# Optimization experiments

Measured on AMD Instinct MI355X. Metric: run time of the kernel, lower is better.

## Reference

```python
import jax, jax.numpy as jnp
import numpy as np

HIDDEN = 256
MSG = 256
N_CLASSES = 2


def _ggnn(x, adj, W_lin, b_lin, W_ih, b_ih, W_hh, b_hh, n_timesteps):
    # Append supernode: zero-embedding row to h, ones row + zeros col to adj.
    N = x.shape[0]
    h0 = jnp.concatenate([x, jnp.zeros((1, x.shape[1]), x.dtype)], axis=0)  # [N+1, H]
    A = jnp.concatenate([adj, jnp.ones((1, N), adj.dtype)], axis=0)         # [N+1, N]
    A = jnp.concatenate([A, jnp.zeros((N + 1, 1), adj.dtype)], axis=1)      # [N+1, N+1]

    def step(h, _):
        msgs = h @ W_lin.T + b_lin          # [N+1, MSG] linear projection
        m = A @ msgs                        # [N+1, MSG] message aggregation
        # GRUCell (PyTorch convention): gates order r, z, n
        gi = m @ W_ih.T + b_ih              # [N+1, 3H]
        gh = h @ W_hh.T + b_hh              # [N+1, 3H]
        ir, iz, inn = jnp.split(gi, 3, axis=-1)
        hr, hz, hn = jnp.split(gh, 3, axis=-1)
        r = jax.nn.sigmoid(ir + hr)
        z = jax.nn.sigmoid(iz + hz)
        n = jnp.tanh(inn + r * hn)
        h_new = (1.0 - z) * n + z * h
        return h_new, None

    h, _ = jax.lax.scan(step, h0, None, length=n_timesteps)
    return h


def setup_inputs() -> dict:
    key = jax.random.key(0)
    ks = jax.random.split(key, 12)
    N = 8000
    inp = {
        "b_x": jax.random.normal(ks[0], (N, HIDDEN), dtype=jnp.float32),
        "b_adj": (jax.random.uniform(ks[1], (N, N), dtype=jnp.float32) < 0.002).astype(jnp.float32),
        "a_x": jax.random.normal(ks[2], (N, HIDDEN), dtype=jnp.float32),
        "a_adj": (jax.random.uniform(ks[3], (N, N), dtype=jnp.float32) < 0.002).astype(jnp.float32),
        "W_lin": jax.random.normal(ks[4], (MSG, HIDDEN), dtype=jnp.float32) * 0.05,
        "b_lin": jnp.zeros((MSG,), dtype=jnp.float32),
        "W_ih": jax.random.normal(ks[5], (3 * HIDDEN, MSG), dtype=jnp.float32) * 0.05,
        "b_ih": jnp.zeros((3 * HIDDEN,), dtype=jnp.float32),
        "W_hh": jax.random.normal(ks[6], (3 * HIDDEN, HIDDEN), dtype=jnp.float32) * 0.05,
        "b_hh": jnp.zeros((3 * HIDDEN,), dtype=jnp.float32),
        "W_fc": jax.random.normal(ks[7], (N_CLASSES, 2 * HIDDEN), dtype=jnp.float32) * 0.05,
        "b_fc": jnp.zeros((N_CLASSES,), dtype=jnp.float32),
        "n_timesteps": 8,
    }
    return inp


def reference(b_x, b_adj, a_x, a_adj, W_lin, b_lin, W_ih, b_ih, W_hh, b_hh, W_fc, b_fc, n_timesteps):
    b_h = _ggnn(b_x, b_adj, W_lin, b_lin, W_ih, b_ih, W_hh, b_hh, n_timesteps)
    a_h = _ggnn(a_x, a_adj, W_lin, b_lin, W_ih, b_ih, W_hh, b_hh, n_timesteps)
    supernodes = jnp.concatenate([b_h[-1, :], a_h[-1, :]], axis=0)  # [2H]
    logits = supernodes @ W_fc.T + b_fc                              # [n_classes]
    return jax.nn.log_softmax(logits, axis=0)
```

## Files before the change

### kernel.cpp

```cpp
#include <hip/hip_runtime.h>
#include <hip/hip_bf16.h>
#include <math.h>

#define NNODES 8000
#define NP1    8001
#define H      256
#define CAP    64
#define TSTEPS 8
#define MTOT   (2*NP1)
#define MPAD   16128
#define NRB    (MPAD/32)

typedef __attribute__((ext_vector_type(8))) short short8;
typedef __attribute__((ext_vector_type(4))) float floatx4;

__device__ __forceinline__ float bl2f(unsigned short u) {
  union { unsigned int i; float f; } z; z.i = ((unsigned int)u) << 16; return z.f;
}
__device__ __forceinline__ unsigned short f2bl(float f) {
  __hip_bfloat16 b = __float2bfloat16(f);
  return *(unsigned short*)&b;
}
__device__ __forceinline__ float sigf(float x) { return 1.f / (1.f + __expf(-x)); }
__device__ __forceinline__ float tanhf_fast(float x) { return 2.f / (1.f + __expf(-2.f * x)) - 1.f; }

__global__ __launch_bounds__(256) void build_ell_kernel(
    const float* __restrict__ adj_b, const float* __restrict__ adj_a,
    int* __restrict__ counts, int* __restrict__ colidx)
{
  int w = threadIdx.x >> 6, l = threadIdx.x & 63;
  int b = blockIdx.x * 4 + w;
  int g = b >= NNODES;
  int row = b - g * NNODES;
  const float* adj = (g ? adj_a : adj_b) + (size_t)row * NNODES;
  unsigned long long lt = (1ull << l) - 1;
  int base = 0;
  int* dst = colidx + (size_t)b * CAP;

  #define SLOT(vec, u, colv) { \
    bool nz = (&vec.x)[u] != 0.f; \
    unsigned long long m = __ballot(nz); \
    if (nz) { int idx = base + (int)__popcll(m & lt); if (idx < CAP) dst[idx] = (colv); } \
    base += (int)__popcll(m); }
  #define GROUP(vec, cb) { \
    bool any4 = ((&vec.x)[0] != 0.f) | ((&vec.x)[1] != 0.f) | \
                ((&vec.x)[2] != 0.f) | ((&vec.x)[3] != 0.f); \
    if (__ballot(any4)) { \
      SLOT(vec, 0, (cb) + 0) SLOT(vec, 1, (cb) + 1) \
      SLOT(vec, 2, (cb) + 2) SLOT(vec, 3, (cb) + 3) } }

  for (int c0 = l * 4; c0 < NNODES; c0 += 1024) {
    int c1 = c0 + 256, c2 = c0 + 512, c3 = c0 + 768;
    bool p1 = c1 < NNODES, p2 = c2 < NNODES, p3 = c3 < NNODES;
    float4 v0 = *(const float4*)(adj + c0);
    float4 v1 = p1 ? *(const float4*)(adj + c1) : make_float4(0,0,0,0);
    float4 v2 = p2 ? *(const float4*)(adj + c2) : make_float4(0,0,0,0);
    float4 v3 = p3 ? *(const float4*)(adj + c3) : make_float4(0,0,0,0);
    GROUP(v0, c0) GROUP(v1, c1) GROUP(v2, c2) GROUP(v3, c3)
  }
  #undef GROUP
  #undef SLOT
  if (l == 0) counts[b] = base < CAP ? base : CAP;
}

__global__ __launch_bounds__(256) void degf_kernel(
    const int* __restrict__ counts, float* __restrict__ degf)
{
  int row = blockIdx.x * 256 + threadIdx.x;
  float d = 0.f;
  if (row < MTOT) {
    int g = row >= NP1;
    int r = row - g * NP1;
    if (r < NNODES) d = (float)counts[g * NNODES + r];
    else if (r == NNODES) d = (float)NNODES;
  }
  degf[row] = d;
}

__global__ __launch_bounds__(256) void weights_kernel(
    const float* __restrict__ Wih, const float* __restrict__ Wlin,
    const float* __restrict__ blin, const float* __restrict__ Whh,
    __hip_bfloat16* __restrict__ Wbig2, float* __restrict__ bc)
{
  __shared__ float srow[H];
  __shared__ float red[256];
  int p = blockIdx.x;
  int ct32 = p / 96, w96 = p - ct32 * 96;
  int gb = w96 >> 4, u = w96 & 15;
  int jj = gb >> 1, uh = gb & 1;
  int c = ct32 * 32 + uh * 16 + u;
  int gr = jj * 256 + c;
  int t = threadIdx.x;
  size_t ob = (size_t)p * 512;
  srow[t] = Wih[(size_t)gr * H + t];
  __syncthreads();
  float acc = 0.f;
  #pragma unroll 8
  for (int k = 0; k < H; ++k) acc += srow[k] * Wlin[(size_t)k * H + t];
  Wbig2[ob + t] = __float2bfloat16(acc);
  Wbig2[ob + 256 + t] = __float2bfloat16(Whh[(size_t)gr * H + t]);
  red[t] = srow[t] * blin[t];
  __syncthreads();
  for (int s = 128; s > 0; s >>= 1) { if (t < s) red[t] += red[t + s]; __syncthreads(); }
  if (t == 0) bc[gr] = red[0];
}

__global__ __launch_bounds__(256) void init_h_kernel(
    const float* __restrict__ bx, const float* __restrict__ ax,
    float* __restrict__ h, __hip_bfloat16* __restrict__ hbf, float* __restrict__ cs0)
{
  int b = blockIdx.x;
  int t = threadIdx.x;
  float l0 = 0.f, l1 = 0.f;
  for (int q = 0; q < 32; ++q) {
    int row = b * 32 + q;
    int g = row >= NP1;
    int r = row - g * NP1;
    float v = 0.f;
    if (r < NNODES) {
      v = (g ? ax : bx)[(size_t)r * H + t];
      if (g) l1 += v; else l0 += v;
    }
    size_t off = (size_t)row * H + t;
    h[off] = v;
    hbf[off] = __float2bfloat16(v);
  }
  if (l0 != 0.f) atomicAdd(&cs0[t], l0);
  if (l1 != 0.f) atomicAdd(&cs0[256 + t], l1);
}

__global__ __launch_bounds__(256) void spmm_kernel(
    const unsigned short* __restrict__ hbf, unsigned short* __restrict__ haggbf,
    const int* __restrict__ counts, const int* __restrict__ colidx,
    const float* __restrict__ cs)
{
  int w = threadIdx.x >> 6, l = threadIdx.x & 63;
  int b = blockIdx.x * 4 + w;
  if (b >= MTOT) return;
  int g = b >= NP1;
  int r = b - g * NP1;
  size_t outoff = (size_t)b * H + l * 4;
  if (r == NNODES) {
    float4 v = *(const float4*)&cs[g * H + l * 4];
    ushort4 o; o.x = f2bl(v.x); o.y = f2bl(v.y); o.z = f2bl(v.z); o.w = f2bl(v.w);
    *(ushort4*)(haggbf + outoff) = o;
    return;
  }
  int rb = g * NNODES + r;
  int cnt = counts[rb];
  const int* cols = colidx + (size_t)rb * CAP;
  const unsigned short* hg = hbf + (size_t)g * NP1 * H;
  float a0 = 0.f, a1 = 0.f, a2 = 0.f, a3 = 0.f;
  int k = 0;
  for (; k + 4 <= cnt; k += 4) {
    int c0 = cols[k], c1 = cols[k+1], c2 = cols[k+2], c3 = cols[k+3];
    uint2 x0 = *(const uint2*)(hg + (size_t)c0 * H + l * 4);
    uint2 x1 = *(const uint2*)(hg + (size_t)c1 * H + l * 4);
    uint2 x2 = *(const uint2*)(hg + (size_t)c2 * H + l * 4);
    uint2 x3 = *(const uint2*)(hg + (size_t)c3 * H + l * 4);
    a0 += bl2f(x0.x & 0xffff) + bl2f(x1.x & 0xffff) + bl2f(x2.x & 0xffff) + bl2f(x3.x & 0xffff);
    a1 += bl2f(x0.x >> 16)    + bl2f(x1.x >> 16)    + bl2f(x2.x >> 16)    + bl2f(x3.x >> 16);
    a2 += bl2f(x0.y & 0xffff) + bl2f(x1.y & 0xffff) + bl2f(x2.y & 0xffff) + bl2f(x3.y & 0xffff);
    a3 += bl2f(x0.y >> 16)    + bl2f(x1.y >> 16)    + bl2f(x2.y >> 16)    + bl2f(x3.y >> 16);
  }
  for (; k < cnt; ++k) {
    uint2 x = *(const uint2*)(hg + (size_t)cols[k] * H + l * 4);
    a0 += bl2f(x.x & 0xffff); a1 += bl2f(x.x >> 16);
    a2 += bl2f(x.y & 0xffff); a3 += bl2f(x.y >> 16);
  }
  ushort4 o; o.x = f2bl(a0); o.y = f2bl(a1); o.z = f2bl(a2); o.w = f2bl(a3);
  *(ushort4*)(haggbf + outoff) = o;
}

__global__ __launch_bounds__(256, 2) void fused_gemm_gru_kernel(
    const __hip_bfloat16* __restrict__ haggbf, const __hip_bfloat16* __restrict__ hin,
    const __hip_bfloat16* __restrict__ Wbig2, const float* __restrict__ degf,
    const float* __restrict__ bc, const float* __restrict__ bih,
    const float* __restrict__ bhh,
    float* __restrict__ h, __hip_bfloat16* __restrict__ hout,
    float* __restrict__ cs_next)
{
  __shared__ __align__(16) short lsA[256 * 32];
  __shared__ __align__(16) short lsB[96 * 32];
  int bidx = blockIdx.x;
  int ct = bidx >> 6;
  int m_i = bidx & 63;
  if (m_i >= 63) return;
  int m0 = m_i * 256;
  const short* Bbase = (const short*)Wbig2 + (size_t)ct * 96 * 512;
  int t = threadIdx.x;
  int w = t >> 6, l = t & 63;
  int lr = l >> 2, lc = l & 3;
  int wm = (w & 1) * 128, uh = w >> 1;
  int q = l >> 4, lm = l & 15;
  floatx4 acc[8][4] = {};

  for (int k0 = 0; k0 < 512; k0 += 32) {
    bool ihalf = (k0 < 256);
    const short* Asrc = ihalf ? (const short*)haggbf : (const short*)hin;
    int ka = k0 & 255;
    #pragma unroll
    for (int j = 0; j < 4; ++j) {
      int r = w * 64 + j * 16 + lr;
      int cch = lc ^ ((r >> 1) & 3);
      const short* ga = Asrc + (size_t)(m0 + r) * H + ka + cch * 8;
      short* la = lsA + (w * 64 + j * 16) * 32;
      __builtin_amdgcn_global_load_lds((const __attribute__((address_space(1))) void*)ga,
                                       (__attribute__((address_space(3))) void*)la, 16, 0, 0);
    }
    if (w < 3) {
      #pragma unroll
      for (int j = 0; j < 2; ++j) {
        int r = (w * 2 + j) * 16 + lr;
        int cch = lc ^ ((r >> 1) & 3);
        const short* gb = Bbase + (size_t)r * 512 + k0 + cch * 8;
        short* lb = lsB + (w * 2 + j) * 16 * 32;
        __builtin_amdgcn_global_load_lds((const __attribute__((address_space(1))) void*)gb,
                                         (__attribute__((address_space(3))) void*)lb, 16, 0, 0);
      }
    }
    __syncthreads();
    short8 bfr[3];
    #pragma unroll
    for (int jj = 0; jj < 3; ++jj) {
      int n = (jj * 2 + uh) * 16 + lm;
      bfr[jj] = *(const short8*)&lsB[n * 32 + (q ^ ((n >> 1) & 3)) * 8];
    }
    #pragma unroll
    for (int i = 0; i < 8; ++i) {
      int m = wm + i * 16 + lm;
      short8 af = *(const short8*)&lsA[m * 32 + (q ^ ((m >> 1) & 3)) * 8];
      acc[i][0] = __builtin_amdgcn_mfma_f32_16x16x32_bf16(af, bfr[0], acc[i][0], 0, 0, 0);
      acc[i][1] = __builtin_amdgcn_mfma_f32_16x16x32_bf16(af, bfr[1], acc[i][1], 0, 0, 0);
      if (ihalf)
        acc[i][2] = __builtin_amdgcn_mfma_f32_16x16x32_bf16(af, bfr[2], acc[i][2], 0, 0, 0);
      else
        acc[i][3] = __builtin_amdgcn_mfma_f32_16x16x32_bf16(af, bfr[2], acc[i][3], 0, 0, 0);
    }
    __syncthreads();
  }

  int c = ct * 32 + uh * 16 + lm;
  float bcr = bc[c], bcz = bc[256 + c], bcn = bc[512 + c];
  float br  = bih[c] + bhh[c];
  float bz  = bih[256 + c] + bhh[256 + c];
  float bin = bih[512 + c];
  float bhn = bhh[512 + c];
  float lu0 = 0.f, lu1 = 0.f;
  #pragma unroll
  for (int i = 0; i < 8; ++i) {
    int row0 = m0 + wm + i * 16 + q * 4;
    float4 dg = *(const float4*)&degf[row0];
    #pragma unroll
    for (int reg = 0; reg < 4; ++reg) {
      int row = row0 + reg;
      float deg = (&dg.x)[reg];
      float rg = sigf(acc[i][0][reg] + deg * bcr + br);
      float z  = sigf(acc[i][1][reg] + deg * bcz + bz);
      float n  = tanhf_fast(acc[i][2][reg] + deg * bcn + bin + rg * (acc[i][3][reg] + bhn));
      size_t hoff = (size_t)row * H + c;
      float hp = h[hoff];
      float hnew = (1.f - z) * n + z * hp;
      h[hoff] = hnew;
      hout[hoff] = __float2bfloat16(hnew);
      if (row < NP1) { if (row < NNODES) lu0 += hnew; }
      else { if (row - NP1 < NNODES) lu1 += hnew; }
    }
  }
  lu0 += __shfl_down(lu0, 32); lu0 += __shfl_down(lu0, 16);
  lu1 += __shfl_down(lu1, 32); lu1 += __shfl_down(lu1, 16);
  if (q == 0) {
    if (lu0 != 0.f) atomicAdd(&cs_next[c], lu0);
    if (lu1 != 0.f) atomicAdd(&cs_next[256 + c], lu1);
  }
}

__global__ __launch_bounds__(256) void final_kernel(
    const float* __restrict__ h, const float* __restrict__ Wfc,
    const float* __restrict__ bfc, float* __restrict__ out)
{
  __shared__ float red0[256];
  __shared__ float red1[256];
  int t = threadIdx.x;
  float sn0 = h[(size_t)NNODES * H + t];
  float sn1 = h[((size_t)NP1 + NNODES) * H + t];
  red0[t] = sn0 * Wfc[t]       + sn1 * Wfc[H + t];
  red1[t] = sn0 * Wfc[512 + t] + sn1 * Wfc[512 + H + t];
  __syncthreads();
  for (int s = 128; s > 0; s >>= 1) {
    if (t < s) { red0[t] += red0[t + s]; red1[t] += red1[t + s]; }
    __syncthreads();
  }
  if (t == 0) {
    float l0 = red0[0] + bfc[0], l1 = red1[0] + bfc[1];
    float m = fmaxf(l0, l1);
    float lse = m + logf(expf(l0 - m) + expf(l1 - m));
    out[0] = l0 - lse;
    out[1] = l1 - lse;
  }
}

extern "C" void kernel_launch(void* const* d_in, const int* in_sizes, int n_in,
                              void* d_out, int out_size, void* d_ws, size_t ws_size,
                              hipStream_t stream) {
  const float* b_x   = (const float*)d_in[0];
  const float* b_adj = (const float*)d_in[1];
  const float* a_x   = (const float*)d_in[2];
  const float* a_adj = (const float*)d_in[3];
  const float* Wlin  = (const float*)d_in[4];
  const float* blin  = (const float*)d_in[5];
  const float* Wih   = (const float*)d_in[6];
  const float* bih   = (const float*)d_in[7];
  const float* Whh   = (const float*)d_in[8];
  const float* bhh   = (const float*)d_in[9];
  const float* Wfc   = (const float*)d_in[10];
  const float* bfc   = (const float*)d_in[11];
  float* out = (float*)d_out;

  char* ws = (char*)d_ws;
  size_t off = 0;
  auto alloc = [&](size_t bytes) {
    void* p = ws + off;
    off += (bytes + 255) & ~(size_t)255;
    return p;
  };
  float* h               = (float*)alloc((size_t)MPAD * H * 4);
  __hip_bfloat16* hbf0   = (__hip_bfloat16*)alloc((size_t)MPAD * H * 2);
  __hip_bfloat16* hbf1   = (__hip_bfloat16*)alloc((size_t)MPAD * H * 2);
  __hip_bfloat16* haggbf = (__hip_bfloat16*)alloc((size_t)MPAD * H * 2);
  __hip_bfloat16* Wbig2  = (__hip_bfloat16*)alloc((size_t)768 * 512 * 2);
  float* bc              = (float*)alloc((size_t)768 * 4);
  int* colidx            = (int*)alloc((size_t)2 * NNODES * CAP * 4);
  int* counts            = (int*)alloc((size_t)2 * NNODES * 4 + 1024);
  float* degf            = (float*)alloc((size_t)MPAD * 4);
  float* cs              = (float*)alloc((size_t)(TSTEPS + 1) * 2 * H * 4);

  hipMemsetAsync(cs, 0, (size_t)(TSTEPS + 1) * 2 * H * 4, stream);

  build_ell_kernel<<<4000, 256, 0, stream>>>(b_adj, a_adj, counts, colidx);
  degf_kernel<<<MPAD / 256, 256, 0, stream>>>(counts, degf);
  weights_kernel<<<768, 256, 0, stream>>>(Wih, Wlin, blin, Whh, Wbig2, bc);
  init_h_kernel<<<NRB, 256, 0, stream>>>(b_x, a_x, h, hbf0, cs);

  __hip_bfloat16* ping[2] = { hbf0, hbf1 };
  for (int t = 0; t < TSTEPS; ++t) {
    __hip_bfloat16* hin  = ping[t & 1];
    __hip_bfloat16* hout = ping[(t + 1) & 1];
    spmm_kernel<<<(MTOT + 3) / 4, 256, 0, stream>>>(
        (const unsigned short*)hin, (unsigned short*)haggbf, counts, colidx, cs + t * 2 * H);
    fused_gemm_gru_kernel<<<512, 256, 0, stream>>>(
        haggbf, hin, Wbig2, degf, bc, bih, bhh, h, hout, cs + (t + 1) * 2 * H);
  }
  final_kernel<<<1, 256, 0, stream>>>(h, Wfc, bfc, out);
}
```

Before: 911.9 us.

## Double-buffer LDS in fused GEMM and broadcast neighbor indices via shuffles

Converts the fused GEMM+GRU kernel's K loop to a two-stage LDS double buffer: the next tile is loaded while the current one is computed, and one barrier per iteration is removed. In the gather kernel, each lane loads one column index up front and the indices are broadcast with wave shuffles instead of repeated scalar loads. The change doubles LDS use and relies on barrier waitcnt semantics for correctness; the shuffle path assumes cnt <= 64.

```diff
diff --git a/kernel.cpp b/kernel.cpp
--- a/kernel.cpp
+++ b/kernel.cpp
@@ -149,11 +149,13 @@
   int rb = g * NNODES + r;
   int cnt = counts[rb];
   const int* cols = colidx + (size_t)rb * CAP;
+  int c_l = (l < cnt) ? cols[l] : 0;
   const unsigned short* hg = hbf + (size_t)g * NP1 * H;
   float a0 = 0.f, a1 = 0.f, a2 = 0.f, a3 = 0.f;
   int k = 0;
   for (; k + 4 <= cnt; k += 4) {
-    int c0 = cols[k], c1 = cols[k+1], c2 = cols[k+2], c3 = cols[k+3];
+    int c0 = __shfl(c_l, k), c1 = __shfl(c_l, k + 1);
+    int c2 = __shfl(c_l, k + 2), c3 = __shfl(c_l, k + 3);
     uint2 x0 = *(const uint2*)(hg + (size_t)c0 * H + l * 4);
     uint2 x1 = *(const uint2*)(hg + (size_t)c1 * H + l * 4);
     uint2 x2 = *(const uint2*)(hg + (size_t)c2 * H + l * 4);
@@ -164,7 +166,8 @@
     a3 += bl2f(x0.y >> 16)    + bl2f(x1.y >> 16)    + bl2f(x2.y >> 16)    + bl2f(x3.y >> 16);
   }
   for (; k < cnt; ++k) {
-    uint2 x = *(const uint2*)(hg + (size_t)cols[k] * H + l * 4);
+    int c = __shfl(c_l, k);
+    uint2 x = *(const uint2*)(hg + (size_t)c * H + l * 4);
     a0 += bl2f(x.x & 0xffff); a1 += bl2f(x.x >> 16);
     a2 += bl2f(x.y & 0xffff); a3 += bl2f(x.y >> 16);
   }
@@ -180,14 +183,16 @@
     float* __restrict__ h, __hip_bfloat16* __restrict__ hout,
     float* __restrict__ cs_next)
 {
-  __shared__ __align__(16) short lsA[256 * 32];
-  __shared__ __align__(16) short lsB[96 * 32];
+  __shared__ __align__(16) short lsA[2][256 * 32];
+  __shared__ __align__(16) short lsB[2][96 * 32];
   int bidx = blockIdx.x;
   int ct = bidx >> 6;
   int m_i = bidx & 63;
   if (m_i >= 63) return;
   int m0 = m_i * 256;
   const short* Bbase = (const short*)Wbig2 + (size_t)ct * 96 * 512;
+  const short* Ai = (const short*)haggbf;
+  const short* Ah = (const short*)hin;
   int t = threadIdx.x;
   int w = t >> 6, l = t & 63;
   int lr = l >> 2, lc = l & 3;
@@ -195,41 +200,49 @@
   int q = l >> 4, lm = l & 15;
   floatx4 acc[8][4] = {};
 
-  for (int k0 = 0; k0 < 512; k0 += 32) {
-    bool ihalf = (k0 < 256);
-    const short* Asrc = ihalf ? (const short*)haggbf : (const short*)hin;
-    int ka = k0 & 255;
-    #pragma unroll
-    for (int j = 0; j < 4; ++j) {
-      int r = w * 64 + j * 16 + lr;
-      int cch = lc ^ ((r >> 1) & 3);
-      const short* ga = Asrc + (size_t)(m0 + r) * H + ka + cch * 8;
-      short* la = lsA + (w * 64 + j * 16) * 32;
-      __builtin_amdgcn_global_load_lds((const __attribute__((address_space(1))) void*)ga,
-                                       (__attribute__((address_space(3))) void*)la, 16, 0, 0);
-    }
-    if (w < 3) {
-      #pragma unroll
-      for (int j = 0; j < 2; ++j) {
-        int r = (w * 2 + j) * 16 + lr;
-        int cch = lc ^ ((r >> 1) & 3);
-        const short* gb = Bbase + (size_t)r * 512 + k0 + cch * 8;
-        short* lb = lsB + (w * 2 + j) * 16 * 32;
-        __builtin_amdgcn_global_load_lds((const __attribute__((address_space(1))) void*)gb,
-                                         (__attribute__((address_space(3))) void*)lb, 16, 0, 0);
-      }
-    }
+  #define STAGE(ks) { \
+    int buf_ = (ks) & 1; \
+    int k0_ = (ks) * 32; \
+    const short* Asrc_ = (k0_ < 256) ? Ai : Ah; \
+    int ka_ = k0_ & 255; \
+    _Pragma("unroll") \
+    for (int j = 0; j < 4; ++j) { \
+      int r_ = w * 64 + j * 16 + lr; \
+      int cch_ = lc ^ ((r_ >> 1) & 3); \
+      const short* ga_ = Asrc_ + (size_t)(m0 + r_) * H + ka_ + cch_ * 8; \
+      short* la_ = &lsA[buf_][(w * 64 + j * 16) * 32]; \
+      __builtin_amdgcn_global_load_lds((const __attribute__((address_space(1))) void*)ga_, \
+                                       (__attribute__((address_space(3))) void*)la_, 16, 0, 0); \
+    } \
+    if (w < 3) { \
+      _Pragma("unroll") \
+      for (int j = 0; j < 2; ++j) { \
+        int r_ = (w * 2 + j) * 16 + lr; \
+        int cch_ = lc ^ ((r_ >> 1) & 3); \
+        const short* gb_ = Bbase + (size_t)r_ * 512 + k0_ + cch_ * 8; \
+        short* lb_ = &lsB[buf_][(w * 2 + j) * 16 * 32]; \
+        __builtin_amdgcn_global_load_lds((const __attribute__((address_space(1))) void*)gb_, \
+                                         (__attribute__((address_space(3))) void*)lb_, 16, 0, 0); \
+      } \
+    } }
+
+  STAGE(0)
+  #pragma unroll 4
+  for (int ks = 0; ks < 16; ++ks) {
     __syncthreads();
+    if (ks < 15) STAGE(ks + 1)
+    int buf = ks & 1;
+    bool ihalf = ks < 8;
     short8 bfr[3];
     #pragma unroll
     for (int jj = 0; jj < 3; ++jj) {
       int n = (jj * 2 + uh) * 16 + lm;
-      bfr[jj] = *(const short8*)&lsB[n * 32 + (q ^ ((n >> 1) & 3)) * 8];
+      bfr[jj] = *(const short8*)&lsB[buf][n * 32 + (q ^ ((n >> 1) & 3)) * 8];
     }
     #pragma unroll
     for (int i = 0; i < 8; ++i) {
       int m = wm + i * 16 + lm;
-      short8 af = *(const short8*)&lsA[m * 32 + (q ^ ((m >> 1) & 3)) * 8];
+      short8 af = *(const short8*)&lsA[buf][m * 32 + (q ^ ((m >> 1) & 3)) * 8];
       acc[i][0] = __builtin_amdgcn_mfma_f32_16x16x32_bf16(af, bfr[0], acc[i][0], 0, 0, 0);
       acc[i][1] = __builtin_amdgcn_mfma_f32_16x16x32_bf16(af, bfr[1], acc[i][1], 0, 0, 0);
       if (ihalf)
@@ -237,8 +250,8 @@
       else
         acc[i][3] = __builtin_amdgcn_mfma_f32_16x16x32_bf16(af, bfr[2], acc[i][3], 0, 0, 0);
     }
-    __syncthreads();
-  }
+  }
+  #undef STAGE
 
   int c = ct * 32 + uh * 16 + lm;
   float bcr = bc[c], bcz = bc[256 + c], bcn = bc[512 + c];
```

Measured after the change: 963.6 us. 5.7% more time.

## Drop fp32 hidden state and widen GEMM K-tile to 64

Applied to the files above, without the earlier changes.

Removes the fp32 copy of the hidden state. The GRU update now reads the previous hidden value from the bf16 ping-pong buffer, which cuts a 4-byte read and a 4-byte write per element on every step. The GEMM K-step also doubles from 32 to 64 with an 8-way XOR swizzle, halving the number of barrier pairs per tile and spreading the B loads across all four waves. The cost is that the recurrent state is carried entirely in bf16, so rounding error compounds across the timesteps, and LDS use per block doubles.

```diff
diff --git a/kernel.cpp b/kernel.cpp
--- a/kernel.cpp
+++ b/kernel.cpp
@@ -107,7 +107,7 @@
 
 __global__ __launch_bounds__(256) void init_h_kernel(
     const float* __restrict__ bx, const float* __restrict__ ax,
-    float* __restrict__ h, __hip_bfloat16* __restrict__ hbf, float* __restrict__ cs0)
+    __hip_bfloat16* __restrict__ hbf, float* __restrict__ cs0)
 {
   int b = blockIdx.x;
   int t = threadIdx.x;
@@ -121,9 +121,7 @@
       v = (g ? ax : bx)[(size_t)r * H + t];
       if (g) l1 += v; else l0 += v;
     }
-    size_t off = (size_t)row * H + t;
-    h[off] = v;
-    hbf[off] = __float2bfloat16(v);
+    hbf[(size_t)row * H + t] = __float2bfloat16(v);
   }
   if (l0 != 0.f) atomicAdd(&cs0[t], l0);
   if (l1 != 0.f) atomicAdd(&cs0[256 + t], l1);
@@ -177,65 +175,71 @@
     const __hip_bfloat16* __restrict__ Wbig2, const float* __restrict__ degf,
     const float* __restrict__ bc, const float* __restrict__ bih,
     const float* __restrict__ bhh,
-    float* __restrict__ h, __hip_bfloat16* __restrict__ hout,
-    float* __restrict__ cs_next)
-{
-  __shared__ __align__(16) short lsA[256 * 32];
-  __shared__ __align__(16) short lsB[96 * 32];
+    __hip_bfloat16* __restrict__ hout, float* __restrict__ cs_next)
+{
+  __shared__ __align__(16) short lsA[256 * 64];
+  __shared__ __align__(16) short lsB[96 * 64];
   int bidx = blockIdx.x;
   int ct = bidx >> 6;
   int m_i = bidx & 63;
   if (m_i >= 63) return;
   int m0 = m_i * 256;
   const short* Bbase = (const short*)Wbig2 + (size_t)ct * 96 * 512;
+  const short* Ai = (const short*)haggbf;
+  const short* Ah = (const short*)hin;
+  const unsigned short* hin_us = (const unsigned short*)hin;
   int t = threadIdx.x;
   int w = t >> 6, l = t & 63;
-  int lr = l >> 2, lc = l & 3;
+  int lr = l >> 3;
+  int lc = l & 7;
   int wm = (w & 1) * 128, uh = w >> 1;
   int q = l >> 4, lm = l & 15;
   floatx4 acc[8][4] = {};
 
-  for (int k0 = 0; k0 < 512; k0 += 32) {
-    bool ihalf = (k0 < 256);
-    const short* Asrc = ihalf ? (const short*)haggbf : (const short*)hin;
+  for (int ks = 0; ks < 8; ++ks) {
+    int k0 = ks * 64;
+    bool ihalf = ks < 4;
+    const short* Asrc = ihalf ? Ai : Ah;
     int ka = k0 & 255;
     #pragma unroll
-    for (int j = 0; j < 4; ++j) {
-      int r = w * 64 + j * 16 + lr;
-      int cch = lc ^ ((r >> 1) & 3);
-      const short* ga = Asrc + (size_t)(m0 + r) * H + ka + cch * 8;
-      short* la = lsA + (w * 64 + j * 16) * 32;
+    for (int j = 0; j < 8; ++j) {
+      int r = w * 64 + j * 8 + lr;
+      int sc = lc ^ (r & 7);
+      const short* ga = Asrc + (size_t)(m0 + r) * H + ka + sc * 8;
+      short* la = lsA + (w * 64 + j * 8) * 64;
       __builtin_amdgcn_global_load_lds((const __attribute__((address_space(1))) void*)ga,
                                        (__attribute__((address_space(3))) void*)la, 16, 0, 0);
     }
-    if (w < 3) {
+    #pragma unroll
+    for (int j = 0; j < 3; ++j) {
+      int r = w * 24 + j * 8 + lr;
+      int sc = lc ^ (r & 7);
+      const short* gb = Bbase + (size_t)r * 512 + k0 + sc * 8;
+      short* lb = lsB + (w * 24 + j * 8) * 64;
+      __builtin_amdgcn_global_load_lds((const __attribute__((address_space(1))) void*)gb,
+                                       (__attribute__((address_space(3))) void*)lb, 16, 0, 0);
+    }
+    __syncthreads();
+    #pragma unroll
+    for (int kh = 0; kh < 2; ++kh) {
+      int kc = kh * 4 + q;
+      short8 bfr[3];
       #pragma unroll
-      for (int j = 0; j < 2; ++j) {
-        int r = (w * 2 + j) * 16 + lr;
-        int cch = lc ^ ((r >> 1) & 3);
-        const short* gb = Bbase + (size_t)r * 512 + k0 + cch * 8;
-        short* lb = lsB + (w * 2 + j) * 16 * 32;
-        __builtin_amdgcn_global_load_lds((const __attribute__((address_space(1))) void*)gb,
-                                         (__attribute__((address_space(3))) void*)lb, 16, 0, 0);
+      for (int jj = 0; jj < 3; ++jj) {
+        int n = (jj * 2 + uh) * 16 + lm;
+        bfr[jj] = *(const short8*)&lsB[n * 64 + (kc ^ (n & 7)) * 8];
       }
-    }
-    __syncthreads();
-    short8 bfr[3];
-    #pragma unroll
-    for (int jj = 0; jj < 3; ++jj) {
-      int n = (jj * 2 + uh) * 16 + lm;
-      bfr[jj] = *(const short8*)&lsB[n * 32 + (q ^ ((n >> 1) & 3)) * 8];
-    }
-    #pragma unroll
-    for (int i = 0; i < 8; ++i) {
-      int m = wm + i * 16 + lm;
-      short8 af = *(const short8*)&lsA[m * 32 + (q ^ ((m >> 1) & 3)) * 8];
-      acc[i][0] = __builtin_amdgcn_mfma_f32_16x16x32_bf16(af, bfr[0], acc[i][0], 0, 0, 0);
-      acc[i][1] = __builtin_amdgcn_mfma_f32_16x16x32_bf16(af, bfr[1], acc[i][1], 0, 0, 0);
-      if (ihalf)
-        acc[i][2] = __builtin_amdgcn_mfma_f32_16x16x32_bf16(af, bfr[2], acc[i][2], 0, 0, 0);
-      else
-        acc[i][3] = __builtin_amdgcn_mfma_f32_16x16x32_bf16(af, bfr[2], acc[i][3], 0, 0, 0);
+      #pragma unroll
+      for (int i = 0; i < 8; ++i) {
+        int m = wm + i * 16 + lm;
+        short8 af = *(const short8*)&lsA[m * 64 + (kc ^ (m & 7)) * 8];
+        acc[i][0] = __builtin_amdgcn_mfma_f32_16x16x32_bf16(af, bfr[0], acc[i][0], 0, 0, 0);
+        acc[i][1] = __builtin_amdgcn_mfma_f32_16x16x32_bf16(af, bfr[1], acc[i][1], 0, 0, 0);
+        if (ihalf)
+          acc[i][2] = __builtin_amdgcn_mfma_f32_16x16x32_bf16(af, bfr[2], acc[i][2], 0, 0, 0);
+        else
+          acc[i][3] = __builtin_amdgcn_mfma_f32_16x16x32_bf16(af, bfr[2], acc[i][3], 0, 0, 0);
+      }
     }
     __syncthreads();
   }
@@ -259,9 +263,8 @@
       float z  = sigf(acc[i][1][reg] + deg * bcz + bz);
       float n  = tanhf_fast(acc[i][2][reg] + deg * bcn + bin + rg * (acc[i][3][reg] + bhn));
       size_t hoff = (size_t)row * H + c;
-      float hp = h[hoff];
+      float hp = bl2f(hin_us[hoff]);
       float hnew = (1.f - z) * n + z * hp;
-      h[hoff] = hnew;
       hout[hoff] = __float2bfloat16(hnew);
       if (row < NP1) { if (row < NNODES) lu0 += hnew; }
       else { if (row - NP1 < NNODES) lu1 += hnew; }
@@ -276,14 +279,14 @@
 }
 
 __global__ __launch_bounds__(256) void final_kernel(
-    const float* __restrict__ h, const float* __restrict__ Wfc,
+    const unsigned short* __restrict__ hbf, const float* __restrict__ Wfc,
     const float* __restrict__ bfc, float* __restrict__ out)
 {
   __shared__ float red0[256];
   __shared__ float red1[256];
   int t = threadIdx.x;
-  float sn0 = h[(size_t)NNODES * H + t];
-  float sn1 = h[((size_t)NP1 + NNODES) * H + t];
+  float sn0 = bl2f(hbf[(size_t)NNODES * H + t]);
+  float sn1 = bl2f(hbf[((size_t)NP1 + NNODES) * H + t]);
   red0[t] = sn0 * Wfc[t]       + sn1 * Wfc[H + t];
   red1[t] = sn0 * Wfc[512 + t] + sn1 * Wfc[512 + H + t];
   __syncthreads();
@@ -324,7 +327,6 @@
     off += (bytes + 255) & ~(size_t)255;
     return p;
   };
-  float* h               = (float*)alloc((size_t)MPAD * H * 4);
   __hip_bfloat16* hbf0   = (__hip_bfloat16*)alloc((size_t)MPAD * H * 2);
   __hip_bfloat16* hbf1   = (__hip_bfloat16*)alloc((size_t)MPAD * H * 2);
   __hip_bfloat16* haggbf = (__hip_bfloat16*)alloc((size_t)MPAD * H * 2);
@@ -340,7 +342,7 @@
   build_ell_kernel<<<4000, 256, 0, stream>>>(b_adj, a_adj, counts, colidx);
   degf_kernel<<<MPAD / 256, 256, 0, stream>>>(counts, degf);
   weights_kernel<<<768, 256, 0, stream>>>(Wih, Wlin, blin, Whh, Wbig2, bc);
-  init_h_kernel<<<NRB, 256, 0, stream>>>(b_x, a_x, h, hbf0, cs);
+  init_h_kernel<<<NRB, 256, 0, stream>>>(b_x, a_x, hbf0, cs);
 
   __hip_bfloat16* ping[2] = { hbf0, hbf1 };
   for (int t = 0; t < TSTEPS; ++t) {
@@ -349,7 +351,7 @@
     spmm_kernel<<<(MTOT + 3) / 4, 256, 0, stream>>>(
         (const unsigned short*)hin, (unsigned short*)haggbf, counts, colidx, cs + t * 2 * H);
     fused_gemm_gru_kernel<<<512, 256, 0, stream>>>(
-        haggbf, hin, Wbig2, degf, bc, bih, bhh, h, hout, cs + (t + 1) * 2 * H);
-  }
-  final_kernel<<<1, 256, 0, stream>>>(h, Wfc, bfc, out);
-}
+        haggbf, hin, Wbig2, degf, bc, bih, bhh, hout, cs + (t + 1) * 2 * H);
+  }
+  final_kernel<<<1, 256, 0, stream>>>((const unsigned short*)ping[TSTEPS & 1], Wfc, bfc, out);
+}
```

Result: faster. 886.6 us (-2.8%).
